# Kernel optimization log

Measured on AMD Instinct MI355X. Metric: run time of the kernel, lower is better.

## Reference

```python
import jax, jax.numpy as jnp
import numpy as np

N = 100_000      # points
DEG = 16         # uniform neighbor count
E = N * DEG      # edges
NB = 4           # radial basis count (n)
MB = 4           # angular basis count (m)
FIN = 8
FOUT = 8
SUPPORT = 2.0    # module-level `support` constant in the original source


def _rbf_linear(nb, x, periodic):
    # evalRBFSeries(..., which='linear', epsilon=1.0): hat functions on [-1,1]
    if periodic:
        spacing = 2.0 / nb
        centroids = jnp.linspace(-1.0, 1.0, nb + 1)[:nb]          # [nb]
        ra = x[None, :] - centroids[:, None]                       # [nb, E]
        d = jnp.minimum(jnp.minimum(jnp.abs(ra), jnp.abs(ra - 2.0)), jnp.abs(ra + 2.0)) / spacing
    else:
        spacing = 2.0 / (nb - 1)
        centroids = jnp.linspace(-1.0, 1.0, nb)
        d = jnp.abs(x[None, :] - centroids[:, None]) / spacing     # [nb, E]
    return jnp.clip(1.0 - d, 0.0, 1.0)


def setup_inputs() -> dict:
    key = jax.random.key(0)
    k1, k2, k3, k4 = jax.random.split(key, 4)
    positions = jax.random.uniform(k1, (N, 2), dtype=jnp.float32)
    features = jax.random.normal(k2, (N, FIN), dtype=jnp.float32)
    # neighbors: DEG per point, never self (avoids zero-distance edges)
    offs = jax.random.randint(k3, (E,), 1, N)
    base = jnp.repeat(jnp.arange(N, dtype=jnp.int32), DEG)
    neighbors = ((base + offs) % N).astype(jnp.int32)
    row_splits = (jnp.arange(N + 1, dtype=jnp.int32) * DEG)
    # glorot_normal for kernel [fout, fin, n, m]
    kernel = jax.random.normal(k4, (FOUT, FIN, NB, MB), dtype=jnp.float32) * np.float32(
        np.sqrt(2.0 / ((FIN + FOUT) * NB * MB)))
    return {"positions": positions, "features": features, "kernel": kernel,
            "neighbors": neighbors, "row_splits": row_splits}


def reference(positions, features, kernel, neighbors, row_splits):
    n_pts = positions.shape[0]
    n_edges = neighbors.shape[0]
    counts = row_splits[1:] - row_splits[:-1]                       # [N]
    seg = jnp.repeat(jnp.arange(n_pts, dtype=jnp.int32), counts,
                     total_repeat_length=n_edges)                   # [E] owning point per edge
    rel = positions[neighbors] - positions[seg]                     # [E, 2]
    r = jnp.linalg.norm(rel, axis=1) / SUPPORT                      # [E]
    theta = jnp.arctan2(rel[:, 1], rel[:, 0])                       # [E]
    c = _rbf_linear(NB, r * 2.0 - 1.0, periodic=False)              # [NB, E]
    f = _rbf_linear(MB, theta / np.float32(np.pi), periodic=True)   # [MB, E]
    M = jnp.einsum('un,vn->nuv', c, f)                              # [E, NB, MB] per-edge outer product
    O = jnp.einsum('unm,ijnm->uij', M, kernel)                      # [E, FOUT, FIN]
    fv = features[neighbors]                                        # [E, FIN]
    FO = jnp.einsum('nij,nj->ni', O, fv)                            # [E, FOUT]
    return jax.ops.segment_sum(FO, seg, num_segments=n_pts)         # [N, FOUT]
```

## Files before the change

kernel.cpp:

```cpp
#include <hip/hip_runtime.h>
#include <math.h>


#define TWO_OVER_PI 0.63661977236758134f

__device__ __forceinline__ float fast_atan2f(float y, float x) {
    float ax = fabsf(x), ay = fabsf(y);
    float mx = fmaxf(ax, ay);
    float mn = fminf(ax, ay);
    mx = fmaxf(mx, 1e-30f);
    float r = mn * __builtin_amdgcn_rcpf(mx);
    float s = r * r;
    float p = -0.0117212f;
    p = fmaf(p, s,  0.05265332f);
    p = fmaf(p, s, -0.11643287f);
    p = fmaf(p, s,  0.19354346f);
    p = fmaf(p, s, -0.33262347f);
    p = fmaf(p, s,  0.99997726f);
    float a = p * r;
    a = (ay > ax) ? (1.57079632679f - a) : a;
    a = (x < 0.0f) ? (3.14159265359f - a) : a;
    return copysignf(a, y);
}

__device__ __forceinline__ void edge_basis(float dx, float dy,
                                           float c[4], float f[4]) {
    float dist = sqrtf(fmaf(dx, dx, dy * dy));
    float tr = dist * 1.5f;
    float theta = fast_atan2f(dy, dx);
    float ta = fmaf(theta, TWO_OVER_PI, 2.0f);
#pragma unroll
    for (int n = 0; n < 4; ++n)
        c[n] = fmaxf(1.0f - fabsf(tr - (float)n), 0.0f);
#pragma unroll
    for (int m = 0; m < 4; ++m) {
        float d = fabsf(ta - (float)m);
        d = fminf(d, 4.0f - d);
        f[m] = fmaxf(1.0f - d, 0.0f);
    }
}

__global__ __launch_bounds__(256) void rbf_kernel(
    const float* __restrict__ positions,
    const float* __restrict__ features,
    const float* __restrict__ kern,
    const int*   __restrict__ neighbors,
    const int*   __restrict__ row_splits,
    float*       __restrict__ out,
    int npts)
{
    __shared__ float Kl[1024];
    {
        const float4* src = (const float4*)kern;
        float4* dst = (float4*)Kl;
        dst[threadIdx.x] = src[threadIdx.x];
    }
    __syncthreads();

    int gt   = blockIdx.x * blockDim.x + threadIdx.x;
    int u    = gt >> 2;
    int sub  = gt & 3;
    int half = sub & 1;
    int eh   = sub >> 1;
    if (u >= npts) return;

    float2 pu = ((const float2*)positions)[u];
    int rs0 = row_splits[u];
    int rs1 = row_splits[u + 1];
    int cnt = rs1 - rs0;

    float g[16][4];
#pragma unroll
    for (int nm = 0; nm < 16; ++nm)
#pragma unroll
        for (int j = 0; j < 4; ++j) g[nm][j] = 0.0f;

    const float2* pos2  = (const float2*)positions;
    const float4* feat4 = (const float4*)features;

    if (cnt == 16) {
        int e0 = rs0 + eh * 8;
        const int4* nb4 = (const int4*)(neighbors + e0);
        int4 nA = nb4[0];
        int4 nB = nb4[1];

        int nbO0 = half ? nA.y : nA.x,  nbP0 = half ? nA.x : nA.y;
        int nbO1 = half ? nA.w : nA.z,  nbP1 = half ? nA.z : nA.w;
        int nbO2 = half ? nB.y : nB.x,  nbP2 = half ? nB.x : nB.y;
        int nbO3 = half ? nB.w : nB.z,  nbP3 = half ? nB.z : nB.w;

        float2 pO0 = pos2[nbO0];
        float2 pO1 = pos2[nbO1];
        float2 pO2 = pos2[nbO2];
        float2 pO3 = pos2[nbO3];
        float4 vO0 = feat4[nbO0 * 2 + half];
        float4 vP0 = feat4[nbP0 * 2 + half];
        float4 vO1 = feat4[nbO1 * 2 + half];
        float4 vP1 = feat4[nbP1 * 2 + half];
        float4 vO2 = feat4[nbO2 * 2 + half];
        float4 vP2 = feat4[nbP2 * 2 + half];
        float4 vO3 = feat4[nbO3 * 2 + half];
        float4 vP3 = feat4[nbP3 * 2 + half];

#define DO_PAIR(pO, vO, vP)                                                   \
        {                                                                     \
            float cO[4], fO[4], cP[4], fP[4];                                 \
            edge_basis(pO.x - pu.x, pO.y - pu.y, cO, fO);                     \
            _Pragma("unroll")                                                 \
            for (int k = 0; k < 4; ++k) {                                     \
                cP[k] = __shfl_xor(cO[k], 1);                                 \
                fP[k] = __shfl_xor(fO[k], 1);                                 \
            }                                                                 \
            float aO[4] = {vO.x, vO.y, vO.z, vO.w};                           \
            float aP[4] = {vP.x, vP.y, vP.z, vP.w};                           \
            _Pragma("unroll")                                                 \
            for (int n = 0; n < 4; ++n)                                       \
                _Pragma("unroll")                                             \
                for (int m = 0; m < 4; ++m) {                                 \
                    float wO = cO[n] * fO[m];                                 \
                    float wP = cP[n] * fP[m];                                 \
                    _Pragma("unroll")                                         \
                    for (int j = 0; j < 4; ++j) {                             \
                        g[n * 4 + m][j] = fmaf(wO, aO[j], g[n * 4 + m][j]);   \
                        g[n * 4 + m][j] = fmaf(wP, aP[j], g[n * 4 + m][j]);   \
                    }                                                         \
                }                                                             \
        }

        DO_PAIR(pO0, vO0, vP0)
        DO_PAIR(pO1, vO1, vP1)
        DO_PAIR(pO2, vO2, vP2)
        DO_PAIR(pO3, vO3, vP3)
#undef DO_PAIR
    } else {
        int c0 = (cnt + 1) >> 1;
        int e0 = rs0 + eh * c0;
        int e1 = (eh == 0) ? (rs0 + c0) : rs1;
        for (int e = e0; e < e1; ++e) {
            int nb = neighbors[e];
            float2 pn = pos2[nb];
            float c[4], f[4];
            edge_basis(pn.x - pu.x, pn.y - pu.y, c, f);
            float4 fv = feat4[nb * 2 + half];
            float fvj[4] = {fv.x, fv.y, fv.z, fv.w};
#pragma unroll
            for (int n = 0; n < 4; ++n)
#pragma unroll
                for (int m = 0; m < 4; ++m) {
                    float w = c[n] * f[m];
#pragma unroll
                    for (int j = 0; j < 4; ++j)
                        g[n * 4 + m][j] = fmaf(w, fvj[j], g[n * 4 + m][j]);
                }
        }
    }

    float o[8];
#pragma unroll
    for (int i = 0; i < 8; ++i) o[i] = 0.0f;

    const float4* K4 = (const float4*)Kl;
#pragma unroll
    for (int i = 0; i < 8; ++i) {
#pragma unroll
        for (int j = 0; j < 4; ++j) {
            int jg = half * 4 + j;
            int base4 = (i * 128 + jg * 16) >> 2;
#pragma unroll
            for (int q = 0; q < 4; ++q) {
                float4 kv = K4[base4 + q];
                o[i] = fmaf(kv.x, g[q * 4 + 0][j], o[i]);
                o[i] = fmaf(kv.y, g[q * 4 + 1][j], o[i]);
                o[i] = fmaf(kv.z, g[q * 4 + 2][j], o[i]);
                o[i] = fmaf(kv.w, g[q * 4 + 3][j], o[i]);
            }
        }
    }

#pragma unroll
    for (int i = 0; i < 8; ++i) {
        o[i] += __shfl_xor(o[i], 1);
        o[i] += __shfl_xor(o[i], 2);
    }

    float2 ov = (sub == 0) ? make_float2(o[0], o[1])
              : (sub == 1) ? make_float2(o[2], o[3])
              : (sub == 2) ? make_float2(o[4], o[5])
                           : make_float2(o[6], o[7]);
    ((float2*)out)[u * 4 + sub] = ov;
}

extern "C" void kernel_launch(void* const* d_in, const int* in_sizes, int n_in,
                              void* d_out, int out_size, void* d_ws, size_t ws_size,
                              hipStream_t stream) {
    const float* positions  = (const float*)d_in[0];
    const float* features   = (const float*)d_in[1];
    const float* kern       = (const float*)d_in[2];
    const int*   neighbors  = (const int*)d_in[3];
    const int*   row_splits = (const int*)d_in[4];
    float* out = (float*)d_out;

    int npts = in_sizes[0] / 2;
    int total = npts * 4;
    int block = 256;
    int grid = (total + block - 1) / block;
    rbf_kernel<<<grid, block, 0, stream>>>(positions, features, kern,
                                           neighbors, row_splits, out, npts);
}
```

Measured before the change: 105.3 us.

## Pack positions and fp16 features into a 32-byte record per point

Adds a pre-pass kernel that writes each point's position and its 8 features, converted to half precision, into one 32-byte workspace record. The main kernel then gathers each neighbor's data with two aligned float4 loads, which replaces separate position and feature gathers. Each of the two edge-half threads now computes the basis for all of its 8 edges itself, rather than exchanging basis values with its partner lane through shuffles. In exchange it adds a second kernel launch and workspace traffic, lowers feature precision to fp16, and doubles the per-thread basis computation.

```diff
diff --git a/kernel.cpp b/kernel.cpp
--- a/kernel.cpp
+++ b/kernel.cpp
@@ -1,4 +1,5 @@
 #include <hip/hip_runtime.h>
+#include <hip/hip_fp16.h>
 #include <math.h>
 
 
@@ -40,7 +41,164 @@
     }
 }
 
-__global__ __launch_bounds__(256) void rbf_kernel(
+__device__ __forceinline__ float2 h2f(float bits) {
+    union { float f; __half2 h; } u;
+    u.f = bits;
+    return make_float2(__low2float(u.h), __high2float(u.h));
+}
+
+__device__ __forceinline__ float h2f_pack(float a, float b) {
+    union { __half2 h; float f; } u;
+    u.h = __floats2half2_rn(a, b);
+    return u.f;
+}
+
+__global__ __launch_bounds__(256) void pack_kernel(
+    const float* __restrict__ positions,
+    const float* __restrict__ features,
+    float4*      __restrict__ packed,
+    int npts)
+{
+    int u = blockIdx.x * blockDim.x + threadIdx.x;
+    if (u >= npts) return;
+    float2 p  = ((const float2*)positions)[u];
+    float4 fa = ((const float4*)features)[u * 2];
+    float4 fb = ((const float4*)features)[u * 2 + 1];
+    float4 q0, q1;
+    q0.x = p.x;
+    q0.y = p.y;
+    q0.z = h2f_pack(fa.x, fa.y);
+    q0.w = h2f_pack(fa.z, fa.w);
+    q1.x = h2f_pack(fb.x, fb.y);
+    q1.y = h2f_pack(fb.z, fb.w);
+    q1.z = 0.0f;
+    q1.w = 0.0f;
+    packed[u * 2]     = q0;
+    packed[u * 2 + 1] = q1;
+}
+
+__global__ __launch_bounds__(256) void rbf_packed_kernel(
+    const float* __restrict__ positions,
+    const float4* __restrict__ packed,
+    const float* __restrict__ kern,
+    const int*   __restrict__ neighbors,
+    const int*   __restrict__ row_splits,
+    float*       __restrict__ out,
+    int npts)
+{
+    __shared__ float Kl[1024];
+    {
+        const float4* src = (const float4*)kern;
+        float4* dst = (float4*)Kl;
+        dst[threadIdx.x] = src[threadIdx.x];
+    }
+    __syncthreads();
+
+    int gt   = blockIdx.x * blockDim.x + threadIdx.x;
+    int u    = gt >> 2;
+    int sub  = gt & 3;
+    int half = sub & 1;
+    int eh   = sub >> 1;
+    if (u >= npts) return;
+
+    float2 pu = ((const float2*)positions)[u];
+    int rs0 = row_splits[u];
+    int rs1 = row_splits[u + 1];
+    int cnt = rs1 - rs0;
+
+    float g[16][4];
+#pragma unroll
+    for (int nm = 0; nm < 16; ++nm)
+#pragma unroll
+        for (int j = 0; j < 4; ++j) g[nm][j] = 0.0f;
+
+#define VISIT(A, C)                                                           \
+    {                                                                         \
+        float c[4], f[4];                                                     \
+        edge_basis(A.x - pu.x, A.y - pu.y, c, f);                             \
+        float2 lo = h2f(half ? C.x : A.z);                                    \
+        float2 hi = h2f(half ? C.y : A.w);                                    \
+        float fvj[4] = {lo.x, lo.y, hi.x, hi.y};                              \
+        _Pragma("unroll")                                                     \
+        for (int n = 0; n < 4; ++n)                                           \
+            _Pragma("unroll")                                                 \
+            for (int m = 0; m < 4; ++m) {                                     \
+                float w = c[n] * f[m];                                        \
+                _Pragma("unroll")                                             \
+                for (int j = 0; j < 4; ++j)                                   \
+                    g[n * 4 + m][j] = fmaf(w, fvj[j], g[n * 4 + m][j]);       \
+            }                                                                 \
+    }
+
+    if (cnt == 16) {
+        int e0 = rs0 + eh * 8;
+        const int4* nb4 = (const int4*)(neighbors + e0);
+        int4 nA = nb4[0];
+        int4 nB = nb4[1];
+#pragma unroll
+        for (int grp = 0; grp < 2; ++grp) {
+            int nb0 = grp ? nB.x : nA.x;
+            int nb1 = grp ? nB.y : nA.y;
+            int nb2 = grp ? nB.z : nA.z;
+            int nb3 = grp ? nB.w : nA.w;
+            float4 A0 = packed[nb0 * 2], C0 = packed[nb0 * 2 + 1];
+            float4 A1 = packed[nb1 * 2], C1 = packed[nb1 * 2 + 1];
+            float4 A2 = packed[nb2 * 2], C2 = packed[nb2 * 2 + 1];
+            float4 A3 = packed[nb3 * 2], C3 = packed[nb3 * 2 + 1];
+            VISIT(A0, C0)
+            VISIT(A1, C1)
+            VISIT(A2, C2)
+            VISIT(A3, C3)
+        }
+    } else {
+        int c0 = (cnt + 1) >> 1;
+        int e0 = rs0 + eh * c0;
+        int e1 = (eh == 0) ? (rs0 + c0) : rs1;
+        for (int e = e0; e < e1; ++e) {
+            int nb = neighbors[e];
+            float4 A = packed[nb * 2];
+            float4 C = packed[nb * 2 + 1];
+            VISIT(A, C)
+        }
+    }
+#undef VISIT
+
+    float o[8];
+#pragma unroll
+    for (int i = 0; i < 8; ++i) o[i] = 0.0f;
+
+    const float4* K4 = (const float4*)Kl;
+#pragma unroll
+    for (int i = 0; i < 8; ++i) {
+#pragma unroll
+        for (int j = 0; j < 4; ++j) {
+            int jg = half * 4 + j;
+            int base4 = (i * 128 + jg * 16) >> 2;
+#pragma unroll
+            for (int q = 0; q < 4; ++q) {
+                float4 kv = K4[base4 + q];
+                o[i] = fmaf(kv.x, g[q * 4 + 0][j], o[i]);
+                o[i] = fmaf(kv.y, g[q * 4 + 1][j], o[i]);
+                o[i] = fmaf(kv.z, g[q * 4 + 2][j], o[i]);
+                o[i] = fmaf(kv.w, g[q * 4 + 3][j], o[i]);
+            }
+        }
+    }
+
+#pragma unroll
+    for (int i = 0; i < 8; ++i) {
+        o[i] += __shfl_xor(o[i], 1);
+        o[i] += __shfl_xor(o[i], 2);
+    }
+
+    float2 ov = (sub == 0) ? make_float2(o[0], o[1])
+              : (sub == 1) ? make_float2(o[2], o[3])
+              : (sub == 2) ? make_float2(o[4], o[5])
+                           : make_float2(o[6], o[7]);
+    ((float2*)out)[u * 4 + sub] = ov;
+}
+
+__global__ __launch_bounds__(256) void rbf_direct_kernel(
     const float* __restrict__ positions,
     const float* __restrict__ features,
     const float* __restrict__ kern,
@@ -78,87 +236,30 @@
     const float2* pos2  = (const float2*)positions;
     const float4* feat4 = (const float4*)features;
 
-    if (cnt == 16) {
-        int e0 = rs0 + eh * 8;
-        const int4* nb4 = (const int4*)(neighbors + e0);
-        int4 nA = nb4[0];
-        int4 nB = nb4[1];
-
-        int nbO0 = half ? nA.y : nA.x,  nbP0 = half ? nA.x : nA.y;
-        int nbO1 = half ? nA.w : nA.z,  nbP1 = half ? nA.z : nA.w;
-        int nbO2 = half ? nB.y : nB.x,  nbP2 = half ? nB.x : nB.y;
-        int nbO3 = half ? nB.w : nB.z,  nbP3 = half ? nB.z : nB.w;
-
-        float2 pO0 = pos2[nbO0];
-        float2 pO1 = pos2[nbO1];
-        float2 pO2 = pos2[nbO2];
-        float2 pO3 = pos2[nbO3];
-        float4 vO0 = feat4[nbO0 * 2 + half];
-        float4 vP0 = feat4[nbP0 * 2 + half];
-        float4 vO1 = feat4[nbO1 * 2 + half];
-        float4 vP1 = feat4[nbP1 * 2 + half];
-        float4 vO2 = feat4[nbO2 * 2 + half];
-        float4 vP2 = feat4[nbP2 * 2 + half];
-        float4 vO3 = feat4[nbO3 * 2 + half];
-        float4 vP3 = feat4[nbP3 * 2 + half];
-
-#define DO_PAIR(pO, vO, vP)                                                   \
-        {                                                                     \
-            float cO[4], fO[4], cP[4], fP[4];                                 \
-            edge_basis(pO.x - pu.x, pO.y - pu.y, cO, fO);                     \
-            _Pragma("unroll")                                                 \
-            for (int k = 0; k < 4; ++k) {                                     \
-                cP[k] = __shfl_xor(cO[k], 1);                                 \
-                fP[k] = __shfl_xor(fO[k], 1);                                 \
-            }                                                                 \
-            float aO[4] = {vO.x, vO.y, vO.z, vO.w};                           \
-            float aP[4] = {vP.x, vP.y, vP.z, vP.w};                           \
-            _Pragma("unroll")                                                 \
-            for (int n = 0; n < 4; ++n)                                       \
-                _Pragma("unroll")                                             \
-                for (int m = 0; m < 4; ++m) {                                 \
-                    float wO = cO[n] * fO[m];                                 \
-                    float wP = cP[n] * fP[m];                                 \
-                    _Pragma("unroll")                                         \
-                    for (int j = 0; j < 4; ++j) {                             \
-                        g[n * 4 + m][j] = fmaf(wO, aO[j], g[n * 4 + m][j]);   \
-                        g[n * 4 + m][j] = fmaf(wP, aP[j], g[n * 4 + m][j]);   \
-                    }                                                         \
-                }                                                             \
-        }
-
-        DO_PAIR(pO0, vO0, vP0)
-        DO_PAIR(pO1, vO1, vP1)
-        DO_PAIR(pO2, vO2, vP2)
-        DO_PAIR(pO3, vO3, vP3)
-#undef DO_PAIR
-    } else {
-        int c0 = (cnt + 1) >> 1;
-        int e0 = rs0 + eh * c0;
-        int e1 = (eh == 0) ? (rs0 + c0) : rs1;
-        for (int e = e0; e < e1; ++e) {
-            int nb = neighbors[e];
-            float2 pn = pos2[nb];
-            float c[4], f[4];
-            edge_basis(pn.x - pu.x, pn.y - pu.y, c, f);
-            float4 fv = feat4[nb * 2 + half];
-            float fvj[4] = {fv.x, fv.y, fv.z, fv.w};
-#pragma unroll
-            for (int n = 0; n < 4; ++n)
-#pragma unroll
-                for (int m = 0; m < 4; ++m) {
-                    float w = c[n] * f[m];
-#pragma unroll
-                    for (int j = 0; j < 4; ++j)
-                        g[n * 4 + m][j] = fmaf(w, fvj[j], g[n * 4 + m][j]);
-                }
-        }
+    int c0 = (cnt + 1) >> 1;
+    int e0 = rs0 + eh * c0;
+    int e1 = (eh == 0) ? (rs0 + c0) : rs1;
+    for (int e = e0; e < e1; ++e) {
+        int nb = neighbors[e];
+        float2 pn = pos2[nb];
+        float c[4], f[4];
+        edge_basis(pn.x - pu.x, pn.y - pu.y, c, f);
+        float4 fv = feat4[nb * 2 + half];
+        float fvj[4] = {fv.x, fv.y, fv.z, fv.w};
+#pragma unroll
+        for (int n = 0; n < 4; ++n)
+#pragma unroll
+            for (int m = 0; m < 4; ++m) {
+                float w = c[n] * f[m];
+#pragma unroll
+                for (int j = 0; j < 4; ++j)
+                    g[n * 4 + m][j] = fmaf(w, fvj[j], g[n * 4 + m][j]);
+            }
     }
 
     float o[8];
 #pragma unroll
     for (int i = 0; i < 8; ++i) o[i] = 0.0f;
-
     const float4* K4 = (const float4*)Kl;
 #pragma unroll
     for (int i = 0; i < 8; ++i) {
@@ -176,13 +277,11 @@
             }
         }
     }
-
 #pragma unroll
     for (int i = 0; i < 8; ++i) {
         o[i] += __shfl_xor(o[i], 1);
         o[i] += __shfl_xor(o[i], 2);
     }
-
     float2 ov = (sub == 0) ? make_float2(o[0], o[1])
               : (sub == 1) ? make_float2(o[2], o[3])
               : (sub == 2) ? make_float2(o[4], o[5])
@@ -204,6 +303,19 @@
     int total = npts * 4;
     int block = 256;
     int grid = (total + block - 1) / block;
-    rbf_kernel<<<grid, block, 0, stream>>>(positions, features, kern,
-                                           neighbors, row_splits, out, npts);
-}
+
+    size_t need = (size_t)npts * 32;
+    if (ws_size >= need) {
+        int pgrid = (npts + block - 1) / block;
+        pack_kernel<<<pgrid, block, 0, stream>>>(positions, features,
+                                                 (float4*)d_ws, npts);
+        rbf_packed_kernel<<<grid, block, 0, stream>>>(positions,
+                                                      (const float4*)d_ws, kern,
+                                                      neighbors, row_splits,
+                                                      out, npts);
+    } else {
+        rbf_direct_kernel<<<grid, block, 0, stream>>>(positions, features, kern,
+                                                      neighbors, row_splits,
+                                                      out, npts);
+    }
+}
```

Result: faster. 102.3 us (-2.9%).
